# Kernel optimization log

Measured on AMD Instinct MI355X. Metric: run time of the kernel, lower is better.

Reference implementation:

```python
import jax, jax.numpy as jnp
import numpy as np

B, L = 4, 2048
D_MODEL, D_STATE, D_CONV, EXPAND = 1024, 16, 4, 2
D_INNER = EXPAND * D_MODEL
DT_RANK = D_MODEL // 16  # mamba-ssm default dt_rank = ceil(d_model/16)


def _mamba(x, in_w, conv_w, conv_b, xproj_w, dt_w, dt_b, A_log, D, out_w):
    # x: [B, L, d_model]; faithful port of mamba_ssm.Mamba forward (slow path math)
    di, ds = A_log.shape
    dt_rank = dt_w.shape[1]
    dc = conv_w.shape[1]
    xz = x @ in_w.T                          # [B, L, 2*di]
    xi, z = jnp.split(xz, 2, axis=-1)
    # causal depthwise conv over time
    xc = jnp.swapaxes(xi, 1, 2)              # [B, di, L]
    xc = jax.lax.conv_general_dilated(
        xc, conv_w[:, None, :], (1,), [(dc - 1, 0)],
        feature_group_count=di, dimension_numbers=('NCH', 'OIH', 'NCH'))
    xc = xc + conv_b[None, :, None]
    xi = jax.nn.silu(jnp.swapaxes(xc, 1, 2))  # [B, L, di]
    proj = xi @ xproj_w.T                    # [B, L, dt_rank + 2*ds]
    dt, Bm, Cm = jnp.split(proj, [dt_rank, dt_rank + ds], axis=-1)
    delta = jax.nn.softplus(dt @ dt_w.T + dt_b)  # [B, L, di]
    A = -jnp.exp(A_log)                      # [di, ds]

    def step(h, t):
        d_t, B_t, C_t, x_t = t               # [B,di],[B,ds],[B,ds],[B,di]
        h = jnp.exp(d_t[:, :, None] * A) * h + (d_t * x_t)[:, :, None] * B_t[:, None, :]
        return h, jnp.einsum('bds,bs->bd', h, C_t)

    xs = (jnp.swapaxes(delta, 0, 1), jnp.swapaxes(Bm, 0, 1),
          jnp.swapaxes(Cm, 0, 1), jnp.swapaxes(xi, 0, 1))
    h0 = jnp.zeros((x.shape[0], di, ds), x.dtype)
    _, ys = jax.lax.scan(step, h0, xs)       # ys: [L, B, di]
    y = jnp.swapaxes(ys, 0, 1) + xi * D
    y = y * jax.nn.silu(z)
    return y @ out_w.T


def setup_inputs() -> dict:
    ks = jax.random.split(jax.random.key(0), 24)

    def p(i, shape, scale=0.02):
        return jax.random.normal(ks[i], shape, jnp.float32) * scale

    inp = {
        'x': jax.random.normal(ks[0], (B, L, D_MODEL), jnp.float32),
        'ln_g': jnp.ones((D_MODEL,), jnp.float32),
        'ln_b': jnp.zeros((D_MODEL,), jnp.float32),
        'merge_w': p(1, (D_MODEL, 2 * D_MODEL)),
        'merge_b': jnp.zeros((D_MODEL,), jnp.float32),
    }
    for j, pre in enumerate(('fwd', 'bwd')):
        o = 2 + j * 8
        inp[pre + '_in_w'] = p(o, (2 * D_INNER, D_MODEL))
        inp[pre + '_conv_w'] = p(o + 1, (D_INNER, D_CONV), 0.3)
        inp[pre + '_conv_b'] = jnp.zeros((D_INNER,), jnp.float32)
        inp[pre + '_xproj_w'] = p(o + 2, (DT_RANK + 2 * D_STATE, D_INNER))
        inp[pre + '_dt_w'] = p(o + 3, (D_INNER, DT_RANK), 0.1)
        inp[pre + '_dt_b'] = -4.0 + p(o + 4, (D_INNER,), 0.5)
        inp[pre + '_A_log'] = jnp.broadcast_to(
            jnp.log(jnp.arange(1, D_STATE + 1, dtype=jnp.float32)), (D_INNER, D_STATE)) + 0.0
        inp[pre + '_D'] = jnp.ones((D_INNER,), jnp.float32)
        inp[pre + '_out_w'] = p(o + 5, (D_MODEL, D_INNER))
    return inp


def reference(x, ln_g, ln_b, merge_w, merge_b,
              fwd_in_w, fwd_conv_w, fwd_conv_b, fwd_xproj_w, fwd_dt_w, fwd_dt_b,
              fwd_A_log, fwd_D, fwd_out_w,
              bwd_in_w, bwd_conv_w, bwd_conv_b, bwd_xproj_w, bwd_dt_w, bwd_dt_b,
              bwd_A_log, bwd_D, bwd_out_w):
    mu = jnp.mean(x, axis=-1, keepdims=True)
    var = jnp.mean(jnp.square(x - mu), axis=-1, keepdims=True)
    xn = (x - mu) / jnp.sqrt(var + 1e-5) * ln_g + ln_b
    y_f = _mamba(xn, fwd_in_w, fwd_conv_w, fwd_conv_b, fwd_xproj_w, fwd_dt_w,
                 fwd_dt_b, fwd_A_log, fwd_D, fwd_out_w)
    y_b = jnp.flip(_mamba(jnp.flip(xn, 1), bwd_in_w, bwd_conv_w, bwd_conv_b,
                          bwd_xproj_w, bwd_dt_w, bwd_dt_b, bwd_A_log, bwd_D,
                          bwd_out_w), 1)
    y = jnp.concatenate([y_f, y_b], axis=-1) @ merge_w.T + merge_b
    return x + y
```

## Files before the change

### kernel.cpp

```cpp
#include <hip/hip_runtime.h>

typedef unsigned short u16;
typedef unsigned int u32;
typedef __attribute__((ext_vector_type(8))) short short8;
typedef __attribute__((ext_vector_type(8))) u16 ushort8v;
typedef __attribute__((ext_vector_type(4))) float float4v;
typedef __attribute__((ext_vector_type(4))) u16 ushort4v;

#define SEQ_L 2048
#define NTOK 8192
#define DMODEL 1024
#define DINNER 2048
#define NCH 32
#define CHL 64

__device__ __forceinline__ float bf2f(u16 v) { return __uint_as_float(((u32)v) << 16); }
__device__ __forceinline__ u16 f2bf(float f) {
    u32 u = __float_as_uint(f);
    return (u16)((u + 0x7FFFu + ((u >> 16) & 1u)) >> 16);
}
__device__ __forceinline__ float loadf(const void* p, size_t i, bool bf) {
    return bf ? bf2f(((const u16*)p)[i]) : ((const float*)p)[i];
}
__device__ __forceinline__ void gl2lds(const void* g, void* l) {
    __builtin_amdgcn_global_load_lds(
        (const __attribute__((address_space(1))) void*)g,
        (__attribute__((address_space(3))) void*)l, 16, 0, 0);
}

__global__ void detect_kernel(const u32* __restrict__ lng, int* __restrict__ flag) {
    if (threadIdx.x == 0) flag[0] = (lng[0] == 0x3F800000u) ? 0 : 1;
}

__global__ void cvt_kernel(const void* __restrict__ in, u16* __restrict__ out,
                           int n4, const int* __restrict__ flag) {
    int i = blockIdx.x * 256 + threadIdx.x;
    if (i >= n4) return;
    bool bf = flag[0] != 0;
    ushort4v o;
    if (bf) {
        o = ((const ushort4v*)in)[i];
    } else {
        float4v v = ((const float4v*)in)[i];
        o.x = f2bf(v.x); o.y = f2bf(v.y); o.z = f2bf(v.z); o.w = f2bf(v.w);
    }
    ((ushort4v*)out)[i] = o;
}

__global__ __launch_bounds__(256) void transpose_ow(const void* __restrict__ ow,
        u16* __restrict__ ot, const int* __restrict__ flag) {
    bool bf = flag[0] != 0;
    __shared__ u16 tile[32][33];
    int k0 = blockIdx.x * 32;
    int j0 = blockIdx.y * 32;
    int tx = threadIdx.x & 31;
    int ty = threadIdx.x >> 5;
    #pragma unroll
    for (int r = 0; r < 4; ++r) {
        int j = ty + r * 8;
        tile[j][tx] = f2bf(loadf(ow, (size_t)(j0 + j) * 2048 + k0 + tx, bf));
    }
    __syncthreads();
    #pragma unroll
    for (int r = 0; r < 4; ++r) {
        int k = ty + r * 8;
        ot[(size_t)(k0 + k) * 1024 + j0 + tx] = tile[tx][k];
    }
}

__global__ __launch_bounds__(256) void ln_kernel(const void* __restrict__ xin,
        const void* __restrict__ g, const void* __restrict__ be,
        u16* __restrict__ xn, const int* __restrict__ flag) {
    bool bf = flag[0] != 0;
    int tok = blockIdx.x;
    int tid = threadIdx.x;
    float v[4];
    if (bf) {
        ushort4v u = ((const ushort4v*)xin)[(size_t)tok * 256 + tid];
        v[0] = bf2f(u.x); v[1] = bf2f(u.y); v[2] = bf2f(u.z); v[3] = bf2f(u.w);
    } else {
        float4v f = ((const float4v*)xin)[(size_t)tok * 256 + tid];
        v[0] = f.x; v[1] = f.y; v[2] = f.z; v[3] = f.w;
    }
    float s = v[0] + v[1] + v[2] + v[3];
    float s2 = v[0]*v[0] + v[1]*v[1] + v[2]*v[2] + v[3]*v[3];
    for (int o = 1; o < 64; o <<= 1) { s += __shfl_xor(s, o); s2 += __shfl_xor(s2, o); }
    __shared__ float red[8];
    int w = tid >> 6;
    if ((tid & 63) == 0) { red[w] = s; red[4 + w] = s2; }
    __syncthreads();
    s = red[0] + red[1] + red[2] + red[3];
    s2 = red[4] + red[5] + red[6] + red[7];
    float mu = s * (1.f / 1024.f);
    float var = s2 * (1.f / 1024.f) - mu * mu;
    float rstd = rsqrtf(var + 1e-5f);
    int base = tid * 4;
    ushort4v o;
    o.x = f2bf((v[0] - mu) * rstd * loadf(g, base + 0, bf) + loadf(be, base + 0, bf));
    o.y = f2bf((v[1] - mu) * rstd * loadf(g, base + 1, bf) + loadf(be, base + 1, bf));
    o.z = f2bf((v[2] - mu) * rstd * loadf(g, base + 2, bf) + loadf(be, base + 2, bf));
    o.w = f2bf((v[3] - mu) * rstd * loadf(g, base + 3, bf) + loadf(be, base + 3, bf));
    ((ushort4v*)xn)[(size_t)tok * 256 + tid] = o;
}

__global__ __launch_bounds__(256) void build_wf(
    const void* __restrict__ dtw, const void* __restrict__ xpw,
    u16* __restrict__ wf, const int* __restrict__ flag)
{
    bool bf = flag[0] != 0;
    int n = blockIdx.x;
    int k0 = threadIdx.x * 8;
    ushort8v o;
    if (n >= DINNER) {
        int r = (n - DINNER) + 64;
        if (bf) {
            o = *(const ushort8v*)((const u16*)xpw + (size_t)r * 2048 + k0);
        } else {
            const float* p = (const float*)xpw + (size_t)r * 2048 + k0;
            #pragma unroll
            for (int j = 0; j < 8; ++j) o[j] = f2bf(p[j]);
        }
    } else {
        float acc[8];
        #pragma unroll
        for (int j = 0; j < 8; ++j) acc[j] = 0.f;
        for (int r = 0; r < 64; ++r) {
            float dw = loadf(dtw, (size_t)n * 64 + r, bf);
            if (bf) {
                ushort8v v = *(const ushort8v*)((const u16*)xpw + (size_t)r * 2048 + k0);
                #pragma unroll
                for (int j = 0; j < 8; ++j) acc[j] = fmaf(dw, bf2f(v[j]), acc[j]);
            } else {
                const float* p = (const float*)xpw + (size_t)r * 2048 + k0;
                #pragma unroll
                for (int j = 0; j < 8; ++j) acc[j] = fmaf(dw, p[j], acc[j]);
            }
        }
        #pragma unroll
        for (int j = 0; j < 8; ++j) o[j] = f2bf(acc[j]);
    }
    *(ushort8v*)(wf + (size_t)n * 2048 + k0) = o;
}

template<int EPI, bool FLIPA>
__global__ __launch_bounds__(256) void gemm_bt(
    const u16* __restrict__ A, int lda,
    const u16* __restrict__ W, int ldw,
    void* __restrict__ Cv, int ldc,
    int M, int N, int K,
    const void* __restrict__ bias, const void* __restrict__ resid,
    const int* __restrict__ flag)
{
    __shared__ u16 As0[128 * 32];
    __shared__ u16 Ws0[128 * 32];
    __shared__ u16 As1[128 * 32];
    __shared__ u16 Ws1[128 * 32];
    bool bf = flag[0] != 0;
    int tid = threadIdx.x;
    int lane = tid & 63;
    int wave = tid >> 6;
    int wm = wave >> 1, wn = wave & 1;
    int m0 = blockIdx.x * 128;
    int n0 = blockIdx.y * 128;
    int l15 = lane & 15;
    int quad = lane >> 4;

    int c0 = tid, c1 = tid + 256;
    int row0 = c0 >> 2, row1 = c1 >> 2;
    int kk0 = ((c0 & 3) ^ ((row0 ^ (row0 >> 1)) & 3)) << 3;
    int kk1 = ((c1 & 3) ^ ((row1 ^ (row1 >> 1)) & 3)) << 3;
    int ar0 = m0 + row0, ar1 = m0 + row1;
    if (FLIPA) {
        int b0 = ar0 >> 11, t0 = ar0 & (SEQ_L - 1); ar0 = (b0 << 11) | (SEQ_L - 1 - t0);
        int b1 = ar1 >> 11, t1 = ar1 & (SEQ_L - 1); ar1 = (b1 << 11) | (SEQ_L - 1 - t1);
    }
    int wr0 = n0 + row0; if (wr0 > N - 1) wr0 = N - 1;
    int wr1 = n0 + row1; if (wr1 > N - 1) wr1 = N - 1;
    const u16* Ag0 = A + (size_t)ar0 * lda + kk0;
    const u16* Ag1 = A + (size_t)ar1 * lda + kk1;
    const u16* Wg0 = W + (size_t)wr0 * ldw + kk0;
    const u16* Wg1 = W + (size_t)wr1 * ldw + kk1;
    int sc0 = c0 * 8, sc1 = c1 * 8;

    int aoff[4], boff[4];
    #pragma unroll
    for (int i = 0; i < 4; ++i) {
        int ra = wm * 64 + i * 16 + l15;
        aoff[i] = ra * 32 + ((quad ^ ((ra ^ (ra >> 1)) & 3)) << 3);
        int rb = wn * 64 + i * 16 + l15;
        boff[i] = rb * 32 + ((quad ^ ((rb ^ (rb >> 1)) & 3)) << 3);
    }

    float4v acc[4][4] = {};
    int nt = K >> 5;

#define STAGE_T(BA, BW, KO) \
    gl2lds(Ag0 + (KO), &BA[sc0]); \
    gl2lds(Ag1 + (KO), &BA[sc1]); \
    gl2lds(Wg0 + (KO), &BW[sc0]); \
    gl2lds(Wg1 + (KO), &BW[sc1]);

#define COMPUTE_T(BA, BW) { \
    short8 af[4], bfr[4]; \
    _Pragma("unroll") \
    for (int i = 0; i < 4; ++i) af[i] = *(const short8*)&BA[aoff[i]]; \
    _Pragma("unroll") \
    for (int j = 0; j < 4; ++j) bfr[j] = *(const short8*)&BW[boff[j]]; \
    _Pragma("unroll") \
    for (int i = 0; i < 4; ++i) { \
        _Pragma("unroll") \
        for (int j = 0; j < 4; ++j) \
            acc[i][j] = __builtin_amdgcn_mfma_f32_16x16x32_bf16(af[i], bfr[j], acc[i][j], 0, 0, 0); \
    } }

#define SYNC_PIPE \
    asm volatile("s_waitcnt vmcnt(0)" ::: "memory"); \
    __builtin_amdgcn_s_barrier();

    STAGE_T(As0, Ws0, 0)
    SYNC_PIPE
    for (int t = 0; t < nt; t += 2) {
        STAGE_T(As1, Ws1, (t + 1) << 5)
        COMPUTE_T(As0, Ws0)
        SYNC_PIPE
        if (t + 2 < nt) { STAGE_T(As0, Ws0, (t + 2) << 5) }
        COMPUTE_T(As1, Ws1)
        SYNC_PIPE
    }
#undef STAGE_T
#undef COMPUTE_T
#undef SYNC_PIPE

    #pragma unroll
    for (int i = 0; i < 4; ++i) {
        #pragma unroll
        for (int j = 0; j < 4; ++j) {
            #pragma unroll
            for (int r = 0; r < 4; ++r) {
                int row = m0 + wm * 64 + i * 16 + quad * 4 + r;
                int col = n0 + wn * 64 + j * 16 + l15;
                if (col < N) {
                    float v = acc[i][j][r];
                    if (EPI == 0) {
                        ((u16*)Cv)[(size_t)row * ldc + col] = f2bf(v);
                    } else if (EPI == 2) {
                        v += loadf(bias, col, bf) + loadf(resid, (size_t)row * DMODEL + col, bf);
                        if (bf) ((u16*)Cv)[(size_t)row * ldc + col] = f2bf(v);
                        else    ((float*)Cv)[(size_t)row * ldc + col] = v;
                    } else if (EPI == 3) {
                        if (col < DINNER) {
                            v += loadf(bias, col, bf);
                            v = fmaxf(v, 0.f) + __logf(1.f + __expf(-fabsf(v)));
                            ((u16*)Cv)[(size_t)row * 4096 + col] = f2bf(v);
                        } else {
                            ((u16*)resid)[(size_t)row * 32 + (col - DINNER)] = f2bf(v);
                        }
                    } else {
                        if (bf) {
                            u16* p = (u16*)Cv + (size_t)row * ldc + col;
                            *p = f2bf(bf2f(*p) + v);
                        } else {
                            float* p = (float*)Cv + (size_t)row * ldc + col;
                            *p = *p + v;
                        }
                    }
                }
            }
        }
    }
}

__global__ __launch_bounds__(256) void conv_kernel(const u16* __restrict__ xz,
        const void* __restrict__ cw, const void* __restrict__ cb,
        u16* __restrict__ xc, const int* __restrict__ flag)
{
    bool bf = flag[0] != 0;
    int gid = blockIdx.x * 256 + threadIdx.x;
    int d = (gid & 255) << 3;
    int tok = gid >> 8;
    int t = tok & (SEQ_L - 1);
    int b = tok >> 11;
    float cwf[32], acc[8];
    if (bf) {
        const u16* p = (const u16*)cw + d * 4;
        #pragma unroll
        for (int r = 0; r < 4; ++r) {
            ushort8v v = *(const ushort8v*)(p + r * 8);
            #pragma unroll
            for (int j = 0; j < 8; ++j) cwf[r * 8 + j] = bf2f(v[j]);
        }
        ushort8v bv = *(const ushort8v*)((const u16*)cb + d);
        #pragma unroll
        for (int j = 0; j < 8; ++j) acc[j] = bf2f(bv[j]);
    } else {
        const float4v* p = (const float4v*)((const float*)cw + d * 4);
        #pragma unroll
        for (int r = 0; r < 8; ++r) {
            float4v v = p[r];
            cwf[r * 4 + 0] = v.x; cwf[r * 4 + 1] = v.y;
            cwf[r * 4 + 2] = v.z; cwf[r * 4 + 3] = v.w;
        }
        const float4v* pb = (const float4v*)((const float*)cb + d);
        float4v b0 = pb[0], b1 = pb[1];
        acc[0] = b0.x; acc[1] = b0.y; acc[2] = b0.z; acc[3] = b0.w;
        acc[4] = b1.x; acc[5] = b1.y; acc[6] = b1.z; acc[7] = b1.w;
    }
    const u16* xp = xz + (((size_t)(b * SEQ_L + t)) << 12) + d;
    #pragma unroll
    for (int k = 0; k < 4; ++k) {
        int tt = t - 3 + k;
        if (tt >= 0) {
            ushort8v xv = *(const ushort8v*)(xp + (long)(k - 3) * 4096);
            #pragma unroll
            for (int j = 0; j < 8; ++j) acc[j] = fmaf(cwf[j * 4 + k], bf2f(xv[j]), acc[j]);
        }
    }
    ushort8v o;
    #pragma unroll
    for (int j = 0; j < 8; ++j) {
        float r = acc[j] / (1.f + __expf(-acc[j]));
        o[j] = f2bf(r);
    }
    *(ushort8v*)(xc + (size_t)tok * DINNER + d) = o;
}


__global__ __launch_bounds__(256) void scan_pass1(
    const u16* __restrict__ xz, const u16* __restrict__ xc,
    const u16* __restrict__ proj, const void* __restrict__ A_log,
    float2* __restrict__ chk, const int* __restrict__ flag)
{
    bool bf = flag[0] != 0;
    int g = blockIdx.x * 256 + threadIdx.x;
    int d = g & (DINNER - 1);
    int c = (g >> 11) & (NCH - 1);
    int b = g >> 16;
    float Ac[16];
    #pragma unroll
    for (int s = 0; s < 16; ++s) Ac[s] = -__expf(loadf(A_log, (size_t)d * 16 + s, bf));
    size_t tok0 = (size_t)b * SEQ_L + c * CHL;
    const u16* dp = xz + tok0 * 4096 + d;
    const u16* xp = xc + tok0 * DINNER + d;
    const u16* bp = proj + tok0 * 32;
    float h[16];
    #pragma unroll
    for (int s = 0; s < 16; ++s) h[s] = 0.f;
    float sd = 0.f;
    for (int t = 0; t < CHL; ++t) {
        float dl = bf2f(*dp);
        float xi = bf2f(*xp);
        ushort8v bv0 = *(const ushort8v*)bp;
        ushort8v bv1 = *(const ushort8v*)(bp + 8);
        float u = dl * xi;
        #pragma unroll
        for (int s = 0; s < 16; ++s) {
            float a = __expf(dl * Ac[s]);
            float Bs = bf2f(s < 8 ? bv0[s] : bv1[s - 8]);
            h[s] = fmaf(a, h[s], u * Bs);
        }
        sd += dl;
        dp += 4096; xp += DINNER; bp += 32;
    }
    size_t base = (size_t)c * 131072 + ((size_t)b << 15) + d;
    #pragma unroll
    for (int s = 0; s < 16; ++s)
        chk[base + (size_t)s * 2048] = make_float2(__expf(Ac[s] * sd), h[s]);
}

__global__ __launch_bounds__(256) void scan_mid(float2* __restrict__ chk) {
    int g = blockIdx.x * 256 + threadIdx.x;
    float hi = 0.f;
    #pragma unroll 4
    for (int c = 0; c < NCH; ++c) {
        float2 v = chk[(size_t)c * 131072 + g];
        chk[(size_t)c * 131072 + g].x = hi;
        hi = fmaf(v.x, hi, v.y);
    }
}

__global__ __launch_bounds__(256) void scan_pass2(
    u16* __restrict__ xz, const u16* __restrict__ xc,
    const u16* __restrict__ proj, const void* __restrict__ A_log,
    const void* __restrict__ Dp, const float2* __restrict__ chk,
    const int* __restrict__ flag)
{
    bool bf = flag[0] != 0;
    int g = blockIdx.x * 256 + threadIdx.x;
    int d = g & (DINNER - 1);
    int c = (g >> 11) & (NCH - 1);
    int b = g >> 16;
    float Ac[16];
    #pragma unroll
    for (int s = 0; s < 16; ++s) Ac[s] = -__expf(loadf(A_log, (size_t)d * 16 + s, bf));
    float Dd = loadf(Dp, d, bf);
    size_t tok0 = (size_t)b * SEQ_L + c * CHL;
    const u16* dp = xz + tok0 * 4096 + d;
    const u16* xp = xc + tok0 * DINNER + d;
    const u16* bp = proj + tok0 * 32;
    u16* zp = xz + tok0 * 4096 + DINNER + d;
    size_t base = (size_t)c * 131072 + ((size_t)b << 15) + d;
    float h[16];
    #pragma unroll
    for (int s = 0; s < 16; ++s) h[s] = chk[base + (size_t)s * 2048].x;
    for (int t = 0; t < CHL; ++t) {
        float dl = bf2f(*dp);
        float xi = bf2f(*xp);
        ushort8v bv0 = *(const ushort8v*)bp;
        ushort8v bv1 = *(const ushort8v*)(bp + 8);
        ushort8v cv0 = *(const ushort8v*)(bp + 16);
        ushort8v cv1 = *(const ushort8v*)(bp + 24);
        float u = dl * xi;
        float y0 = 0.f, y1 = 0.f;
        #pragma unroll
        for (int s = 0; s < 16; ++s) {
            float a = __expf(dl * Ac[s]);
            float Bs = bf2f(s < 8 ? bv0[s] : bv1[s - 8]);
            float Cs = bf2f(s < 8 ? cv0[s] : cv1[s - 8]);
            h[s] = fmaf(a, h[s], u * Bs);
            if (s & 1) y1 = fmaf(h[s], Cs, y1); else y0 = fmaf(h[s], Cs, y0);
        }
        float y = y0 + y1 + xi * Dd;
        float z = bf2f(*zp);
        *zp = f2bf(y * (z / (1.f + __expf(-z))));
        dp += 4096; xp += DINNER; bp += 32; zp += 4096;
    }
}

extern "C" void kernel_launch(void* const* d_in, const int* in_sizes, int n_in,
                              void* d_out, int out_size, void* d_ws, size_t ws_size,
                              hipStream_t stream) {
    (void)in_sizes; (void)n_in; (void)out_size;
    const void* x = d_in[0];
    const void* ln_g = d_in[1];
    const void* ln_be = d_in[2];
    const void* merge_w = d_in[3];
    const void* merge_b = d_in[4];
    const void* in_w[2]   = {d_in[5],  d_in[14]};
    const void* conv_w[2] = {d_in[6],  d_in[15]};
    const void* conv_b[2] = {d_in[7],  d_in[16]};
    const void* xproj_w[2]= {d_in[8],  d_in[17]};
    const void* dt_w[2]   = {d_in[9],  d_in[18]};
    const void* dt_bias[2]= {d_in[10], d_in[19]};
    const void* A_log[2]  = {d_in[11], d_in[20]};
    const void* Dp[2]     = {d_in[12], d_in[21]};
    const void* out_w[2]  = {d_in[13], d_in[22]};

    char* wsb = (char*)d_ws;
    size_t off = 0;
    auto alloc = [&](size_t bytes) -> void* {
        void* p = wsb + off; off += (bytes + 255) & ~(size_t)255; return p;
    };
    int* flag     = (int*)alloc(256);
    u16* xzb      = (u16*)alloc((size_t)NTOK * 4096 * 2);
    u16* xcb      = (u16*)alloc((size_t)NTOK * 2048 * 2);
    u16* projb    = (u16*)alloc((size_t)NTOK * 32 * 2);
    float2* chk   = (float2*)alloc((size_t)NCH * 131072 * 8);
    u16* wf       = (u16*)alloc((size_t)2080 * 2048 * 2);
    u16* wof[2]   = {(u16*)alloc((size_t)1024 * 2048 * 2),
                     (u16*)alloc((size_t)1024 * 2048 * 2)};
    u16* xn       = (u16*)alloc((size_t)NTOK * DMODEL * 2);
    u16* w_mgc    = (u16*)alloc((size_t)1024 * 2048 * 2);
    u16* outT     = (u16*)alloc((size_t)2048 * 1024 * 2);
    if (off > ws_size) return;

    u16* w_in = (u16*)chk;

    detect_kernel<<<1, 64, 0, stream>>>((const u32*)ln_g, flag);
    ln_kernel<<<dim3(NTOK), 256, 0, stream>>>(x, ln_g, ln_be, xn, flag);

    auto cvt = [&](const void* src, u16* dst, int n) {
        cvt_kernel<<<dim3(n / 1024), 256, 0, stream>>>(src, dst, n / 4, flag);
    };

    cvt(merge_w, w_mgc, 1024 * 2048);
    for (int dd = 0; dd < 2; ++dd) {
        transpose_ow<<<dim3(64, 32), 256, 0, stream>>>(out_w[dd], outT, flag);
        gemm_bt<0,false><<<dim3(8, 16), 256, 0, stream>>>(
            w_mgc + dd * 1024, 2048, outT, 1024, wof[dd], 2048, 1024, 2048, 1024,
            nullptr, nullptr, flag);
    }

    for (int dd = 0; dd < 2; ++dd) {
        cvt(in_w[dd], w_in, 4096 * 1024);
        if (dd == 0)
            gemm_bt<0,false><<<dim3(64,32), 256, 0, stream>>>(xn, 1024, w_in, 1024, xzb, 4096, NTOK, 4096, 1024, nullptr, nullptr, flag);
        else
            gemm_bt<0,true><<<dim3(64,32), 256, 0, stream>>>(xn, 1024, w_in, 1024, xzb, 4096, NTOK, 4096, 1024, nullptr, nullptr, flag);
        conv_kernel<<<dim3((NTOK * DINNER / 8) / 256), 256, 0, stream>>>(xzb, conv_w[dd], conv_b[dd], xcb, flag);
        build_wf<<<dim3(2080), 256, 0, stream>>>(dt_w[dd], xproj_w[dd], wf, flag);
        gemm_bt<3,false><<<dim3(64,17), 256, 0, stream>>>(xcb, 2048, wf, 2048, xzb, 4096, NTOK, 2080, 2048, dt_bias[dd], projb, flag);
        scan_pass1<<<dim3(1024), 256, 0, stream>>>(xzb, xcb, projb, A_log[dd], chk, flag);
        scan_mid<<<dim3(512), 256, 0, stream>>>(chk);
        scan_pass2<<<dim3(1024), 256, 0, stream>>>(xzb, xcb, projb, A_log[dd], Dp[dd], chk, flag);
        if (dd == 0)
            gemm_bt<2,false><<<dim3(64,8), 256, 0, stream>>>(xzb + DINNER, 4096, wof[0], 2048, d_out, 1024, NTOK, 1024, 2048, merge_b, x, flag);
        else
            gemm_bt<5,true><<<dim3(64,8), 256, 0, stream>>>(xzb + DINNER, 4096, wof[1], 2048, d_out, 1024, NTOK, 1024, 2048, nullptr, nullptr, flag);
    }
}
```

Baseline: 1.290 ms.

## Deepen GEMM LDS pipeline to four stages with partial vmcnt waits

Replaces the double-buffered LDS staging in the bf16 MFMA GEMM with a four-slot ring buffer. Loads are issued three tiles ahead, and the wait uses vmcnt(12) rather than vmcnt(0), so global-to-LDS transfers overlap more with compute. The cost is LDS use doubling to 64 KB per block, which may cut occupancy, plus two barriers per k-step.

```diff
diff --git a/kernel.cpp b/kernel.cpp
--- a/kernel.cpp
+++ b/kernel.cpp
@@ -151,10 +151,7 @@
     const void* __restrict__ bias, const void* __restrict__ resid,
     const int* __restrict__ flag)
 {
-    __shared__ u16 As0[128 * 32];
-    __shared__ u16 Ws0[128 * 32];
-    __shared__ u16 As1[128 * 32];
-    __shared__ u16 Ws1[128 * 32];
+    __shared__ u16 S[4][2][128 * 32];
     bool bf = flag[0] != 0;
     int tid = threadIdx.x;
     int lane = tid & 63;
@@ -194,18 +191,21 @@
     float4v acc[4][4] = {};
     int nt = K >> 5;
 
-#define STAGE_T(BA, BW, KO) \
-    gl2lds(Ag0 + (KO), &BA[sc0]); \
-    gl2lds(Ag1 + (KO), &BA[sc1]); \
-    gl2lds(Wg0 + (KO), &BW[sc0]); \
-    gl2lds(Wg1 + (KO), &BW[sc1]);
-
-#define COMPUTE_T(BA, BW) { \
+#define STAGE_R(RB, KO) { \
+    u16* la_ = &S[RB][0][0]; u16* lw_ = &S[RB][1][0]; \
+    gl2lds(Ag0 + (KO), la_ + sc0); \
+    gl2lds(Ag1 + (KO), la_ + sc1); \
+    gl2lds(Wg0 + (KO), lw_ + sc0); \
+    gl2lds(Wg1 + (KO), lw_ + sc1); }
+
+#define COMPUTE_R(RB) { \
+    const u16* ap_ = &S[RB][0][0]; \
+    const u16* wp_ = &S[RB][1][0]; \
     short8 af[4], bfr[4]; \
     _Pragma("unroll") \
-    for (int i = 0; i < 4; ++i) af[i] = *(const short8*)&BA[aoff[i]]; \
+    for (int i = 0; i < 4; ++i) af[i] = *(const short8*)(ap_ + aoff[i]); \
     _Pragma("unroll") \
-    for (int j = 0; j < 4; ++j) bfr[j] = *(const short8*)&BW[boff[j]]; \
+    for (int j = 0; j < 4; ++j) bfr[j] = *(const short8*)(wp_ + boff[j]); \
     _Pragma("unroll") \
     for (int i = 0; i < 4; ++i) { \
         _Pragma("unroll") \
@@ -213,23 +213,38 @@
             acc[i][j] = __builtin_amdgcn_mfma_f32_16x16x32_bf16(af[i], bfr[j], acc[i][j], 0, 0, 0); \
     } }
 
-#define SYNC_PIPE \
-    asm volatile("s_waitcnt vmcnt(0)" ::: "memory"); \
-    __builtin_amdgcn_s_barrier();
-
-    STAGE_T(As0, Ws0, 0)
-    SYNC_PIPE
-    for (int t = 0; t < nt; t += 2) {
-        STAGE_T(As1, Ws1, (t + 1) << 5)
-        COMPUTE_T(As0, Ws0)
-        SYNC_PIPE
-        if (t + 2 < nt) { STAGE_T(As0, Ws0, (t + 2) << 5) }
-        COMPUTE_T(As1, Ws1)
-        SYNC_PIPE
-    }
-#undef STAGE_T
-#undef COMPUTE_T
-#undef SYNC_PIPE
+#define WAITV(N) asm volatile("s_waitcnt vmcnt(" #N ")" ::: "memory");
+#define BARRIER { __builtin_amdgcn_s_barrier(); asm volatile("" ::: "memory"); }
+
+    STAGE_R(0, 0)
+    STAGE_R(1, 32)
+    STAGE_R(2, 64)
+    int t = 0;
+    for (; t < nt - 3; ++t) {
+        int rb = t & 3;
+        STAGE_R((t + 3) & 3, (t + 3) << 5)
+        WAITV(12)
+        BARRIER
+        COMPUTE_R(rb)
+        BARRIER
+    }
+    WAITV(8)
+    BARRIER
+    COMPUTE_R(t & 3)
+    BARRIER
+    ++t;
+    WAITV(4)
+    BARRIER
+    COMPUTE_R(t & 3)
+    BARRIER
+    ++t;
+    WAITV(0)
+    BARRIER
+    COMPUTE_R(t & 3)
+#undef STAGE_R
+#undef COMPUTE_R
+#undef WAITV
+#undef BARRIER
 
     #pragma unroll
     for (int i = 0; i < 4; ++i) {
```

Result: no change. 1.285 ms (-0.4%).

## Add 128x256-tile triple-buffered MFMA GEMM for in_proj and dt/x projections

Applied to the files above, without the earlier changes.

Introduces a new GEMM kernel with a 128x256 output tile per block, in which each wave owns a 128x64 strip. It uses a three-stage LDS ring filled by direct global-to-LDS loads with XOR swizzling and explicit vmcnt waits. The kernel replaces the 128x128 double-buffered GEMM for the in_proj and the fused dt/xproj GEMMs, aiming to raise operand reuse per LDS load and to overlap loads with MFMA more deeply. The cost is more LDS and more accumulator registers per block, and the 2080-wide GEMM now rounds up to 2304 columns of wasted tile work.

```diff
diff --git a/kernel.cpp b/kernel.cpp
--- a/kernel.cpp
+++ b/kernel.cpp
@@ -27,6 +27,9 @@
         (const __attribute__((address_space(1))) void*)g,
         (__attribute__((address_space(3))) void*)l, 16, 0, 0);
 }
+
+#define GWAITV(N) asm volatile("s_waitcnt vmcnt(" #N ")" ::: "memory");
+#define GBAR { __builtin_amdgcn_s_barrier(); asm volatile("" ::: "memory"); }
 
 __global__ void detect_kernel(const u32* __restrict__ lng, int* __restrict__ flag) {
     if (threadIdx.x == 0) flag[0] = (lng[0] == 0x3F800000u) ? 0 : 1;
@@ -143,6 +146,128 @@
 }
 
 template<int EPI, bool FLIPA>
+__global__ __launch_bounds__(256, 2) void gemm256(
+    const u16* __restrict__ A, int lda,
+    const u16* __restrict__ W, int ldw,
+    void* __restrict__ Cv, int ldc,
+    int M, int N, int K,
+    const void* __restrict__ bias, const void* __restrict__ resid,
+    const int* __restrict__ flag)
+{
+    __shared__ u16 S[3 * 12288];
+    bool bf = flag[0] != 0;
+    int tid = threadIdx.x;
+    int lane = tid & 63;
+    int wn = tid >> 6;
+    int m0 = blockIdx.x * 128;
+    int n0 = blockIdx.y * 256;
+    int l15 = lane & 15;
+    int quad = lane >> 4;
+
+    const u16* gp[6];
+    int lo[6];
+    #pragma unroll
+    for (int q = 0; q < 6; ++q) {
+        int c = tid + q * 256;
+        lo[q] = c * 8;
+        if (c < 512) {
+            int r = c >> 2, ch = c & 3;
+            int kel = (ch ^ ((r ^ (r >> 1)) & 3)) << 3;
+            int ar = m0 + r;
+            if (FLIPA) { int b0 = ar >> 11, t0 = ar & (SEQ_L - 1); ar = (b0 << 11) | (SEQ_L - 1 - t0); }
+            gp[q] = A + (size_t)ar * lda + kel;
+        } else {
+            int cb = c - 512;
+            int r = cb >> 2, ch = cb & 3;
+            int kel = (ch ^ ((r ^ (r >> 1)) & 3)) << 3;
+            int wr = n0 + r; if (wr > N - 1) wr = N - 1;
+            gp[q] = W + (size_t)wr * ldw + kel;
+        }
+    }
+
+    int aoff[8], boff[4];
+    #pragma unroll
+    for (int i = 0; i < 8; ++i) {
+        int ra = i * 16 + l15;
+        aoff[i] = ra * 32 + ((quad ^ ((ra ^ (ra >> 1)) & 3)) << 3);
+    }
+    #pragma unroll
+    for (int j = 0; j < 4; ++j) {
+        int rb = wn * 64 + j * 16 + l15;
+        boff[j] = 4096 + rb * 32 + ((quad ^ ((rb ^ (rb >> 1)) & 3)) << 3);
+    }
+
+    float4v acc[8][4] = {};
+    int nt = K >> 5;
+
+#define STG(SL, KO) { u16* lb_ = &S[(SL) * 12288]; \
+    _Pragma("unroll") \
+    for (int q_ = 0; q_ < 6; ++q_) gl2lds(gp[q_] + (KO), lb_ + lo[q_]); }
+
+#define CMP(SL) { const u16* sb_ = &S[(SL) * 12288]; \
+    short8 af[8], bfr[4]; \
+    _Pragma("unroll") \
+    for (int i = 0; i < 8; ++i) af[i] = *(const short8*)(sb_ + aoff[i]); \
+    _Pragma("unroll") \
+    for (int j = 0; j < 4; ++j) bfr[j] = *(const short8*)(sb_ + boff[j]); \
+    _Pragma("unroll") \
+    for (int i = 0; i < 8; ++i) { \
+        _Pragma("unroll") \
+        for (int j = 0; j < 4; ++j) \
+            acc[i][j] = __builtin_amdgcn_mfma_f32_16x16x32_bf16(af[i], bfr[j], acc[i][j], 0, 0, 0); \
+    } }
+
+    STG(0, 0)
+    STG(1, 32)
+    int sl = 0;
+    for (int t = 0; t < nt - 2; ++t) {
+        int sp = sl + 2; if (sp >= 3) sp -= 3;
+        STG(sp, (t + 2) << 5)
+        GWAITV(12)
+        GBAR
+        CMP(sl)
+        GBAR
+        ++sl; if (sl == 3) sl = 0;
+    }
+    GWAITV(6)
+    GBAR
+    CMP(sl)
+    GBAR
+    ++sl; if (sl == 3) sl = 0;
+    GWAITV(0)
+    GBAR
+    CMP(sl)
+#undef STG
+#undef CMP
+
+    #pragma unroll
+    for (int i = 0; i < 8; ++i) {
+        #pragma unroll
+        for (int j = 0; j < 4; ++j) {
+            #pragma unroll
+            for (int r = 0; r < 4; ++r) {
+                int row = m0 + i * 16 + quad * 4 + r;
+                int col = n0 + wn * 64 + j * 16 + l15;
+                if (col < N) {
+                    float v = acc[i][j][r];
+                    if (EPI == 0) {
+                        ((u16*)Cv)[(size_t)row * ldc + col] = f2bf(v);
+                    } else if (EPI == 3) {
+                        if (col < DINNER) {
+                            v += loadf(bias, col, bf);
+                            v = fmaxf(v, 0.f) + __logf(1.f + __expf(-fabsf(v)));
+                            ((u16*)Cv)[(size_t)row * 4096 + col] = f2bf(v);
+                        } else {
+                            ((u16*)resid)[(size_t)row * 32 + (col - DINNER)] = f2bf(v);
+                        }
+                    }
+                }
+            }
+        }
+    }
+}
+
+template<int EPI, bool FLIPA>
 __global__ __launch_bounds__(256) void gemm_bt(
     const u16* __restrict__ A, int lda,
     const u16* __restrict__ W, int ldw,
@@ -247,14 +372,6 @@
                         v += loadf(bias, col, bf) + loadf(resid, (size_t)row * DMODEL + col, bf);
                         if (bf) ((u16*)Cv)[(size_t)row * ldc + col] = f2bf(v);
                         else    ((float*)Cv)[(size_t)row * ldc + col] = v;
-                    } else if (EPI == 3) {
-                        if (col < DINNER) {
-                            v += loadf(bias, col, bf);
-                            v = fmaxf(v, 0.f) + __logf(1.f + __expf(-fabsf(v)));
-                            ((u16*)Cv)[(size_t)row * 4096 + col] = f2bf(v);
-                        } else {
-                            ((u16*)resid)[(size_t)row * 32 + (col - DINNER)] = f2bf(v);
-                        }
                     } else {
                         if (bf) {
                             u16* p = (u16*)Cv + (size_t)row * ldc + col;
@@ -323,7 +440,6 @@
     }
     *(ushort8v*)(xc + (size_t)tok * DINNER + d) = o;
 }
-
 
 __global__ __launch_bounds__(256) void scan_pass1(
     const u16* __restrict__ xz, const u16* __restrict__ xc,
@@ -483,12 +599,12 @@
     for (int dd = 0; dd < 2; ++dd) {
         cvt(in_w[dd], w_in, 4096 * 1024);
         if (dd == 0)
-            gemm_bt<0,false><<<dim3(64,32), 256, 0, stream>>>(xn, 1024, w_in, 1024, xzb, 4096, NTOK, 4096, 1024, nullptr, nullptr, flag);
+            gemm256<0,false><<<dim3(64,16), 256, 0, stream>>>(xn, 1024, w_in, 1024, xzb, 4096, NTOK, 4096, 1024, nullptr, nullptr, flag);
         else
-            gemm_bt<0,true><<<dim3(64,32), 256, 0, stream>>>(xn, 1024, w_in, 1024, xzb, 4096, NTOK, 4096, 1024, nullptr, nullptr, flag);
+            gemm256<0,true><<<dim3(64,16), 256, 0, stream>>>(xn, 1024, w_in, 1024, xzb, 4096, NTOK, 4096, 1024, nullptr, nullptr, flag);
         conv_kernel<<<dim3((NTOK * DINNER / 8) / 256), 256, 0, stream>>>(xzb, conv_w[dd], conv_b[dd], xcb, flag);
         build_wf<<<dim3(2080), 256, 0, stream>>>(dt_w[dd], xproj_w[dd], wf, flag);
-        gemm_bt<3,false><<<dim3(64,17), 256, 0, stream>>>(xcb, 2048, wf, 2048, xzb, 4096, NTOK, 2080, 2048, dt_bias[dd], projb, flag);
+        gemm256<3,false><<<dim3(64,9), 256, 0, stream>>>(xcb, 2048, wf, 2048, xzb, 4096, NTOK, 2080, 2048, dt_bias[dd], projb, flag);
         scan_pass1<<<dim3(1024), 256, 0, stream>>>(xzb, xcb, projb, A_log[dd], chk, flag);
         scan_mid<<<dim3(512), 256, 0, stream>>>(chk);
         scan_pass2<<<dim3(1024), 256, 0, stream>>>(xzb, xcb, projb, A_log[dd], Dp[dd], chk, flag);
```

New measurement: 1.248 ms. -3.2%, faster.

## Add 256x256 tile GEMM kernel for in-proj and fused dt/x-proj GEMMs

Applied to the files above, without the earlier changes.

Introduces a new 512-thread GEMM with 256x256 output tiles, a BK=64 double-buffered LDS pipeline built on direct global-to-LDS loads with XOR swizzling, split wait/barrier phases and raised MFMA priority. It replaces the 128x128 kernel for the large in_proj GEMM and for the fused dt/x_proj GEMM. The larger tiles give more reuse per LDS load and issue fewer loads per FLOP. In exchange they use more registers and LDS and launch fewer blocks, and the N=2080 case wastes a mostly empty final tile column.

```diff
diff --git a/kernel.cpp b/kernel.cpp
--- a/kernel.cpp
+++ b/kernel.cpp
@@ -27,6 +27,9 @@
         (const __attribute__((address_space(1))) void*)g,
         (__attribute__((address_space(3))) void*)l, 16, 0, 0);
 }
+
+#define GWAITV(N) asm volatile("s_waitcnt vmcnt(" #N ")" ::: "memory");
+#define GBAR { __builtin_amdgcn_s_barrier(); asm volatile("" ::: "memory"); }
 
 __global__ void detect_kernel(const u32* __restrict__ lng, int* __restrict__ flag) {
     if (threadIdx.x == 0) flag[0] = (lng[0] == 0x3F800000u) ? 0 : 1;
@@ -143,6 +146,144 @@
 }
 
 template<int EPI, bool FLIPA>
+__global__ __launch_bounds__(512, 2) void gemm2x(
+    const u16* __restrict__ A, int lda,
+    const u16* __restrict__ W, int ldw,
+    void* __restrict__ Cv, int ldc,
+    int M, int N, int K,
+    const void* __restrict__ bias, const void* __restrict__ resid,
+    const int* __restrict__ flag)
+{
+    __shared__ u16 S[2][2][16384];
+    bool bf = flag[0] != 0;
+    int tid = threadIdx.x;
+    int lane = tid & 63;
+    int wave = tid >> 6;
+    int wm = wave >> 2;
+    int wn = wave & 3;
+    int m0 = blockIdx.x * 256;
+    int n0 = blockIdx.y * 256;
+    int l15 = lane & 15;
+    int quad = lane >> 4;
+
+    int rloc = tid >> 3;
+    int kk = ((tid & 7) ^ (rloc & 7)) << 3;
+    const u16* Ag[4];
+    const u16* Wg[4];
+    #pragma unroll
+    for (int rb = 0; rb < 4; ++rb) {
+        int ar = m0 + rb * 64 + rloc;
+        if (FLIPA) { int b0 = ar >> 11, t0 = ar & (SEQ_L - 1); ar = (b0 << 11) | (SEQ_L - 1 - t0); }
+        Ag[rb] = A + (size_t)ar * lda + kk;
+        int wr = n0 + rb * 64 + rloc; if (wr > N - 1) wr = N - 1;
+        Wg[rb] = W + (size_t)wr * ldw + kk;
+    }
+
+    int s3 = l15 & 7;
+    int colk[2];
+    #pragma unroll
+    for (int ks = 0; ks < 2; ++ks)
+        colk[ks] = ((((ks ^ (s3 >> 2)) << 2) | (quad ^ (s3 & 3))) << 3);
+    int abase = wm * 8192 + l15 * 64;
+    int bbase = wn * 4096 + l15 * 64;
+
+    float4v acc[8][4] = {};
+    int nt = K >> 6;
+
+#define STA(B, RB, KO) gl2lds(Ag[RB] + (KO), &S[B][0][((RB) * 512 + tid) * 8]);
+#define STB(B, RB, KO) gl2lds(Wg[RB] + (KO), &S[B][1][((RB) * 512 + tid) * 8]);
+
+    STA(0, 0, 0) STA(0, 2, 0)
+    STB(0, 0, 0) STB(0, 1, 0)
+    STB(0, 2, 0) STB(0, 3, 0)
+    STA(0, 1, 0) STA(0, 3, 0)
+
+    for (int t = 0; t < nt; ++t) {
+        int cb = t & 1, nb = cb ^ 1;
+        int ko = (t + 1) << 6;
+        bool stg = (t + 1) < nt;
+        const u16* sa = &S[cb][0][0];
+        const u16* sb = &S[cb][1][0];
+
+        GWAITV(2)
+        GBAR
+        if (stg) { STA(nb, 0, ko) STA(nb, 2, ko) }
+        short8 a0[4][2];
+        #pragma unroll
+        for (int i = 0; i < 4; ++i)
+            #pragma unroll
+            for (int ks = 0; ks < 2; ++ks)
+                a0[i][ks] = *(const short8*)(sa + abase + i * 1024 + colk[ks]);
+        if (stg) { STB(nb, 0, ko) STB(nb, 1, ko) }
+        short8 bbf[4][2];
+        #pragma unroll
+        for (int j = 0; j < 4; ++j)
+            #pragma unroll
+            for (int ks = 0; ks < 2; ++ks)
+                bbf[j][ks] = *(const short8*)(sb + bbase + j * 1024 + colk[ks]);
+        __builtin_amdgcn_s_setprio(1);
+        #pragma unroll
+        for (int i = 0; i < 4; ++i)
+            #pragma unroll
+            for (int j = 0; j < 4; ++j)
+                #pragma unroll
+                for (int ks = 0; ks < 2; ++ks)
+                    acc[i][j] = __builtin_amdgcn_mfma_f32_16x16x32_bf16(a0[i][ks], bbf[j][ks], acc[i][j], 0, 0, 0);
+        __builtin_amdgcn_s_setprio(0);
+        if (stg) {
+            STB(nb, 2, ko) STB(nb, 3, ko)
+            GWAITV(6)
+        } else {
+            GWAITV(0)
+        }
+        GBAR
+        #pragma unroll
+        for (int i = 0; i < 4; ++i)
+            #pragma unroll
+            for (int ks = 0; ks < 2; ++ks)
+                a0[i][ks] = *(const short8*)(sa + abase + (i + 4) * 1024 + colk[ks]);
+        if (stg) { STA(nb, 1, ko) STA(nb, 3, ko) }
+        __builtin_amdgcn_s_setprio(1);
+        #pragma unroll
+        for (int i = 0; i < 4; ++i)
+            #pragma unroll
+            for (int j = 0; j < 4; ++j)
+                #pragma unroll
+                for (int ks = 0; ks < 2; ++ks)
+                    acc[i + 4][j] = __builtin_amdgcn_mfma_f32_16x16x32_bf16(a0[i][ks], bbf[j][ks], acc[i + 4][j], 0, 0, 0);
+        __builtin_amdgcn_s_setprio(0);
+    }
+#undef STA
+#undef STB
+
+    #pragma unroll
+    for (int i = 0; i < 8; ++i) {
+        #pragma unroll
+        for (int j = 0; j < 4; ++j) {
+            #pragma unroll
+            for (int r = 0; r < 4; ++r) {
+                int row = m0 + wm * 128 + i * 16 + quad * 4 + r;
+                int col = n0 + wn * 64 + j * 16 + l15;
+                if (col < N) {
+                    float v = acc[i][j][r];
+                    if (EPI == 0) {
+                        ((u16*)Cv)[(size_t)row * ldc + col] = f2bf(v);
+                    } else if (EPI == 3) {
+                        if (col < DINNER) {
+                            v += loadf(bias, col, bf);
+                            v = fmaxf(v, 0.f) + __logf(1.f + __expf(-fabsf(v)));
+                            ((u16*)Cv)[(size_t)row * 4096 + col] = f2bf(v);
+                        } else {
+                            ((u16*)resid)[(size_t)row * 32 + (col - DINNER)] = f2bf(v);
+                        }
+                    }
+                }
+            }
+        }
+    }
+}
+
+template<int EPI, bool FLIPA>
 __global__ __launch_bounds__(256) void gemm_bt(
     const u16* __restrict__ A, int lda,
     const u16* __restrict__ W, int ldw,
@@ -247,14 +388,6 @@
                         v += loadf(bias, col, bf) + loadf(resid, (size_t)row * DMODEL + col, bf);
                         if (bf) ((u16*)Cv)[(size_t)row * ldc + col] = f2bf(v);
                         else    ((float*)Cv)[(size_t)row * ldc + col] = v;
-                    } else if (EPI == 3) {
-                        if (col < DINNER) {
-                            v += loadf(bias, col, bf);
-                            v = fmaxf(v, 0.f) + __logf(1.f + __expf(-fabsf(v)));
-                            ((u16*)Cv)[(size_t)row * 4096 + col] = f2bf(v);
-                        } else {
-                            ((u16*)resid)[(size_t)row * 32 + (col - DINNER)] = f2bf(v);
-                        }
                     } else {
                         if (bf) {
                             u16* p = (u16*)Cv + (size_t)row * ldc + col;
@@ -323,7 +456,6 @@
     }
     *(ushort8v*)(xc + (size_t)tok * DINNER + d) = o;
 }
-
 
 __global__ __launch_bounds__(256) void scan_pass1(
     const u16* __restrict__ xz, const u16* __restrict__ xc,
@@ -483,12 +615,12 @@
     for (int dd = 0; dd < 2; ++dd) {
         cvt(in_w[dd], w_in, 4096 * 1024);
         if (dd == 0)
-            gemm_bt<0,false><<<dim3(64,32), 256, 0, stream>>>(xn, 1024, w_in, 1024, xzb, 4096, NTOK, 4096, 1024, nullptr, nullptr, flag);
+            gemm2x<0,false><<<dim3(32,16), 512, 0, stream>>>(xn, 1024, w_in, 1024, xzb, 4096, NTOK, 4096, 1024, nullptr, nullptr, flag);
         else
-            gemm_bt<0,true><<<dim3(64,32), 256, 0, stream>>>(xn, 1024, w_in, 1024, xzb, 4096, NTOK, 4096, 1024, nullptr, nullptr, flag);
+            gemm2x<0,true><<<dim3(32,16), 512, 0, stream>>>(xn, 1024, w_in, 1024, xzb, 4096, NTOK, 4096, 1024, nullptr, nullptr, flag);
         conv_kernel<<<dim3((NTOK * DINNER / 8) / 256), 256, 0, stream>>>(xzb, conv_w[dd], conv_b[dd], xcb, flag);
         build_wf<<<dim3(2080), 256, 0, stream>>>(dt_w[dd], xproj_w[dd], wf, flag);
-        gemm_bt<3,false><<<dim3(64,17), 256, 0, stream>>>(xcb, 2048, wf, 2048, xzb, 4096, NTOK, 2080, 2048, dt_bias[dd], projb, flag);
+        gemm2x<3,false><<<dim3(32,9), 512, 0, stream>>>(xcb, 2048, wf, 2048, xzb, 4096, NTOK, 2080, 2048, dt_bias[dd], projb, flag);
         scan_pass1<<<dim3(1024), 256, 0, stream>>>(xzb, xcb, projb, A_log[dd], chk, flag);
         scan_mid<<<dim3(512), 256, 0, stream>>>(chk);
         scan_pass2<<<dim3(1024), 256, 0, stream>>>(xzb, xcb, projb, A_log[dd], Dp[dd], chk, flag);
```

Result: no change. 1.277 ms (-1.0%).
